# Kernel optimization log

Hardware: AMD Instinct MI355X
Metric: run time of the kernel (lower is better)

## Reference

```python
import jax, jax.numpy as jnp
import numpy as np

N_NODES = 50000
N_EDGES = 800000
IN_FEATS = 128
HIDDEN = 128
DNN_H = 256
N_CLASSES = 40


def setup_inputs() -> dict:
    key = jax.random.key(0)
    ks = jax.random.split(key, 12)
    features = jax.random.normal(ks[0], (N_NODES, IN_FEATS), dtype=jnp.float32)
    src = jax.random.randint(ks[1], (N_EDGES,), 0, N_NODES, dtype=jnp.int32)
    dst = jax.random.randint(ks[2], (N_EDGES,), 0, N_NODES, dtype=jnp.int32)
    def lin(k, fi, fo):
        s = 1.0 / np.sqrt(fi)
        return jax.random.uniform(k, (fi, fo), jnp.float32, -s, s)
    W1 = lin(ks[3], IN_FEATS, HIDDEN)
    b1 = jnp.zeros((HIDDEN,), jnp.float32)
    W2 = lin(ks[4], HIDDEN, HIDDEN)
    b2 = jnp.zeros((HIDDEN,), jnp.float32)
    Wd1 = lin(ks[5], HIDDEN, DNN_H)
    bd1 = jnp.zeros((DNN_H,), jnp.float32)
    Wd2 = lin(ks[6], DNN_H, N_CLASSES)
    bd2 = jnp.zeros((N_CLASSES,), jnp.float32)
    return {"features": features, "src": src, "dst": dst,
            "W1": W1, "b1": b1, "W2": W2, "b2": b2,
            "Wd1": Wd1, "bd1": bd1, "Wd2": Wd2, "bd2": bd2}


def _graph_conv(x, src, dst, W, b):
    # dgl GraphConv, norm='both': D_out^{-1/2} -> sum-aggregate -> D_in^{-1/2} -> linear -> relu
    ones = jnp.ones((src.shape[0],), x.dtype)
    deg_out = jax.ops.segment_sum(ones, src, num_segments=N_NODES)
    deg_in = jax.ops.segment_sum(ones, dst, num_segments=N_NODES)
    inv_sqrt_out = jax.lax.rsqrt(jnp.maximum(deg_out, 1.0))  # clamp zero-degree to 1 like dgl
    inv_sqrt_in = jax.lax.rsqrt(jnp.maximum(deg_in, 1.0))
    x = x * inv_sqrt_out[:, None]
    h = jax.ops.segment_sum(x[src], dst, num_segments=N_NODES)  # [N, d] sparse SpMM
    h = h * inv_sqrt_in[:, None]
    return jax.nn.relu(h @ W + b)


def reference(features, src, dst, W1, b1, W2, b2, Wd1, bd1, Wd2, bd2):
    h = _graph_conv(features, src, dst, W1, b1)   # dropout = identity (eval)
    h = _graph_conv(h, src, dst, W2, b2)
    # DNN: Linear -> LeakyReLU(0.01) -> (dropout identity), x2
    h = jax.nn.leaky_relu(h @ Wd1 + bd1, negative_slope=0.01)
    h = jax.nn.leaky_relu(h @ Wd2 + bd2, negative_slope=0.01)
    return h
```

## Files before the change

### kernel.cpp

```cpp
#include <hip/hip_runtime.h>


#define SCAN_B 256

typedef __attribute__((ext_vector_type(8))) short short8v;
typedef __attribute__((ext_vector_type(4))) float f32x4;

__global__ void k_scanA(const int* __restrict__ deg_in, int* __restrict__ incl,
                        int* __restrict__ bsum, int N) {
    __shared__ int s[SCAN_B];
    int t = threadIdx.x, i = blockIdx.x * SCAN_B + t;
    int v = (i < N) ? deg_in[i] : 0;
    s[t] = v; __syncthreads();
    for (int o = 1; o < SCAN_B; o <<= 1) {
        int x = (t >= o) ? s[t - o] : 0;
        __syncthreads();
        s[t] += x;
        __syncthreads();
    }
    if (i < N) incl[i] = s[t];
    if (t == SCAN_B - 1) bsum[blockIdx.x] = s[t];
}

__global__ void k_scanB(int* __restrict__ bsum, int NB) {
    __shared__ int s[SCAN_B];
    int t = threadIdx.x;
    int v = (t < NB) ? bsum[t] : 0;
    s[t] = v; __syncthreads();
    for (int o = 1; o < SCAN_B; o <<= 1) {
        int x = (t >= o) ? s[t - o] : 0;
        __syncthreads();
        s[t] += x;
        __syncthreads();
    }
    if (t < NB) bsum[t] = s[t] - v;
}

__global__ void k_scanC(const int* __restrict__ deg_in, const int* __restrict__ deg_out,
                        int* __restrict__ row_ptr, const int* __restrict__ bsum,
                        float* __restrict__ inv_in, float* __restrict__ inv_out,
                        int N, int E) {
    int t = threadIdx.x, i = blockIdx.x * SCAN_B + t;
    if (i < N) {
        int di = deg_in[i];
        row_ptr[i] = row_ptr[i] - di + bsum[blockIdx.x];
        inv_in[i]  = rsqrtf(fmaxf((float)di, 1.0f));
        inv_out[i] = rsqrtf(fmaxf((float)deg_out[i], 1.0f));
    }
    if (i == 0) row_ptr[N] = E;
}

__global__ void k_scatter3(const int* __restrict__ src, const int* __restrict__ dst,
                           const int* __restrict__ row_ptr, const int* __restrict__ rank,
                           const float* __restrict__ inv_out,
                           int2* __restrict__ edges, int E) {
    int i = blockIdx.x * blockDim.x + threadIdx.x;
    if (i < E) {
        int s = src[i];
        int2 p;
        p.x = s;
        p.y = __float_as_int(inv_out[s]);
        edges[row_ptr[dst[i]] + rank[i]] = p;
    }
}

__global__ void k_gather2(const float* __restrict__ X, const int2* __restrict__ edges,
                          const int* __restrict__ row_ptr, const float* __restrict__ inv_in,
                          const float* __restrict__ bias, float* __restrict__ Y, int N) {
    int lane = threadIdx.x & 31;
    int row = blockIdx.x * 8 + (threadIdx.x >> 5);
    if (row >= N) return;
    int rs = row_ptr[row], re = row_ptr[row + 1];
    float4 acc = {0.f, 0.f, 0.f, 0.f};
    int e = rs;
    #define LDROW(s) (*reinterpret_cast<const float4*>(&X[(size_t)(s) * 128 + lane * 4]))
    for (; e + 4 <= re; e += 4) {
        int2 p0 = edges[e], p1 = edges[e + 1], p2 = edges[e + 2], p3 = edges[e + 3];
        float4 x0 = LDROW(p0.x), x1 = LDROW(p1.x), x2 = LDROW(p2.x), x3 = LDROW(p3.x);
        float c0 = __int_as_float(p0.y), c1 = __int_as_float(p1.y);
        float c2 = __int_as_float(p2.y), c3 = __int_as_float(p3.y);
        acc.x += c0 * x0.x + c1 * x1.x + c2 * x2.x + c3 * x3.x;
        acc.y += c0 * x0.y + c1 * x1.y + c2 * x2.y + c3 * x3.y;
        acc.z += c0 * x0.z + c1 * x1.z + c2 * x2.z + c3 * x3.z;
        acc.w += c0 * x0.w + c1 * x1.w + c2 * x2.w + c3 * x3.w;
    }
    for (; e < re; ++e) {
        int2 p = edges[e];
        float c = __int_as_float(p.y);
        float4 xv = LDROW(p.x);
        acc.x += c * xv.x; acc.y += c * xv.y; acc.z += c * xv.z; acc.w += c * xv.w;
    }
    #undef LDROW
    float si = inv_in[row];
    float4 b4 = *reinterpret_cast<const float4*>(&bias[lane * 4]);
    float4 o;
    o.x = fmaxf(fmaf(acc.x, si, b4.x), 0.f);
    o.y = fmaxf(fmaf(acc.y, si, b4.y), 0.f);
    o.z = fmaxf(fmaf(acc.z, si, b4.z), 0.f);
    o.w = fmaxf(fmaf(acc.w, si, b4.w), 0.f);
    *reinterpret_cast<float4*>(&Y[(size_t)row * 128 + lane * 4]) = o;
}

__device__ inline unsigned short bf16_rne(float f) {
    unsigned int u = __float_as_uint(f);
    u += 0x7fffu + ((u >> 16) & 1u);
    return (unsigned short)(u >> 16);
}

__device__ inline void split1(float a, unsigned short& h, unsigned short& l) {
    unsigned short hh = bf16_rne(a);
    float hf = __uint_as_float((unsigned int)hh << 16);
    l = bf16_rne(a - hf);
    h = hh;
}

template<int K, int N, int ACT, bool DEG>
__global__ __launch_bounds__(256) void k_gemm_mfma(const float* __restrict__ A,
                                                   const float* __restrict__ W,
                                                   const float* __restrict__ bias,
                                                   float* __restrict__ C, int M,
                                                   const int* __restrict__ src,
                                                   const int* __restrict__ dst,
                                                   int* __restrict__ deg_out,
                                                   int* __restrict__ deg_in,
                                                   int* __restrict__ rank, int E, int epb,
                                                   int gmm, int degb) {
    __shared__ unsigned short Bh[64 * K], Bl[64 * K];
    __shared__ unsigned short Ah[128 * 32], Al[128 * 32];

    int t = threadIdx.x;
    int m0, cb;
    if (DEG) {
        int bid = blockIdx.x;
        if (bid < degb) {
            int base = bid * epb;
            int end = min(E, base + epb);
            for (int i = base + t; i < end; i += 256) {
                atomicAdd(&deg_out[src[i]], 1);
                rank[i] = atomicAdd(&deg_in[dst[i]], 1);
            }
            return;
        }
        int tile = bid - degb;
        m0 = (tile % gmm) * 128;
        cb = (tile / gmm) * 64;
    } else {
        m0 = blockIdx.x * 128;
        cb = blockIdx.y * 64;
    }

    {
        int c = t & 63;
        int kb = (t >> 6) * (K / 4);
        bool cok = (N % 64 == 0) || (cb + c < N);
        for (int j = 0; j < K / 4; ++j) {
            int k = kb + j;
            float v = cok ? W[(size_t)k * N + cb + c] : 0.f;
            unsigned short hi, lo; split1(v, hi, lo);
            int byte = (c * 2 * K + 2 * k) ^ ((c & 7) << 4);
            Bh[byte >> 1] = hi;
            Bl[byte >> 1] = lo;
        }
    }

    f32x4 acc[4][2];
    #pragma unroll
    for (int i = 0; i < 4; ++i)
        #pragma unroll
        for (int j = 0; j < 2; ++j)
            acc[i][j] = (f32x4){0.f, 0.f, 0.f, 0.f};

    int lane = t & 63;
    int wave = t >> 6;
    int wm = wave >> 1, wn = wave & 1;
    int lr = lane & 15, lg = lane >> 4;

    for (int kt = 0; kt < K / 32; ++kt) {
        __syncthreads();
        #pragma unroll
        for (int i = 0; i < 4; ++i) {
            int g = i * 256 + t;
            int r = g >> 3;
            int kq = (g & 7) * 4;
            int gr = m0 + r;
            float4 v = {0.f, 0.f, 0.f, 0.f};
            if (gr < M) v = *reinterpret_cast<const float4*>(&A[(size_t)gr * K + kt * 32 + kq]);
            ushort4 h4, l4;
            split1(v.x, h4.x, l4.x);
            split1(v.y, h4.y, l4.y);
            split1(v.z, h4.z, l4.z);
            split1(v.w, h4.w, l4.w);
            int byte = (r * 64 + 2 * kq) ^ ((r & 7) << 4);
            *reinterpret_cast<ushort4*>(&Ah[byte >> 1]) = h4;
            *reinterpret_cast<ushort4*>(&Al[byte >> 1]) = l4;
        }
        __syncthreads();

        short8v bhf[2], blf[2];
        #pragma unroll
        for (int nf = 0; nf < 2; ++nf) {
            int c = wn * 32 + nf * 16 + lr;
            int byte = (c * 2 * K + 2 * (kt * 32 + lg * 8)) ^ ((c & 7) << 4);
            bhf[nf] = *reinterpret_cast<const short8v*>(&Bh[byte >> 1]);
            blf[nf] = *reinterpret_cast<const short8v*>(&Bl[byte >> 1]);
        }
        #pragma unroll
        for (int mf = 0; mf < 4; ++mf) {
            int r = wm * 64 + mf * 16 + lr;
            int byte = (r * 64 + 2 * (lg * 8)) ^ ((r & 7) << 4);
            short8v ahf = *reinterpret_cast<const short8v*>(&Ah[byte >> 1]);
            short8v alf = *reinterpret_cast<const short8v*>(&Al[byte >> 1]);
            #pragma unroll
            for (int nf = 0; nf < 2; ++nf) {
                acc[mf][nf] = __builtin_amdgcn_mfma_f32_16x16x32_bf16(ahf, bhf[nf], acc[mf][nf], 0, 0, 0);
                acc[mf][nf] = __builtin_amdgcn_mfma_f32_16x16x32_bf16(ahf, blf[nf], acc[mf][nf], 0, 0, 0);
                acc[mf][nf] = __builtin_amdgcn_mfma_f32_16x16x32_bf16(alf, bhf[nf], acc[mf][nf], 0, 0, 0);
            }
        }
    }

    #pragma unroll
    for (int mf = 0; mf < 4; ++mf) {
        #pragma unroll
        for (int nf = 0; nf < 2; ++nf) {
            int col = cb + wn * 32 + nf * 16 + lr;
            if ((N % 64 != 0) && col >= N) continue;
            float bv = (ACT < 2) ? bias[col] : 0.f;
            #pragma unroll
            for (int rg = 0; rg < 4; ++rg) {
                int row = m0 + wm * 64 + mf * 16 + lg * 4 + rg;
                if (row < M) {
                    float v = acc[mf][nf][rg];
                    if (ACT == 0) v = fmaxf(v + bv, 0.f);
                    else if (ACT == 1) { v += bv; v = (v > 0.f) ? v : 0.01f * v; }
                    C[(size_t)row * N + col] = v;
                }
            }
        }
    }
}

extern "C" void kernel_launch(void* const* d_in, const int* in_sizes, int n_in,
                              void* d_out, int out_size, void* d_ws, size_t ws_size,
                              hipStream_t stream) {
    const float* feat = (const float*)d_in[0];
    const int*   src  = (const int*)d_in[1];
    const int*   dst  = (const int*)d_in[2];
    const float* W1   = (const float*)d_in[3];
    const float* b1   = (const float*)d_in[4];
    const float* W2   = (const float*)d_in[5];
    const float* b2   = (const float*)d_in[6];
    const float* Wd1  = (const float*)d_in[7];
    const float* bd1  = (const float*)d_in[8];
    const float* Wd2  = (const float*)d_in[9];
    const float* bd2  = (const float*)d_in[10];
    float* out = (float*)d_out;

    const int N = in_sizes[0] / 128;
    const int E = in_sizes[1];

    char* ws = (char*)d_ws;
    size_t off = 0;
    auto alloc = [&](size_t bytes) -> void* {
        void* p = ws + off;
        off += (bytes + 255) & ~(size_t)255;
        return p;
    };
    int* deg_out  = (int*)alloc((size_t)N * 4);
    int* deg_in   = (int*)alloc((size_t)N * 4);
    int* row_ptr  = (int*)alloc((size_t)(N + 1) * 4);
    int* bsum     = (int*)alloc(SCAN_B * 4);
    int* rank     = (int*)alloc((size_t)E * 4);
    int2* edges   = (int2*)alloc((size_t)E * 8);
    float* inv_out = (float*)alloc((size_t)N * 4);
    float* inv_in  = (float*)alloc((size_t)N * 4);
    float* bufA = (float*)alloc((size_t)N * 128 * 4);
    float* bufB = (float*)alloc((size_t)N * 128 * 4);
    float* hd   = (float*)alloc((size_t)N * 256 * 4);

    size_t zspan = (char*)deg_in + (size_t)N * 4 - (char*)deg_out;
    hipMemsetAsync(deg_out, 0, zspan, stream);

    int gE = (E + 255) / 256;
    int gN = (N + SCAN_B - 1) / SCAN_B;
    int gG = (N + 7) / 8;
    int gMM = (N + 127) / 128;

    const int DEGB = 512;
    int epb = (E + DEGB - 1) / DEGB;
    k_gemm_mfma<128, 128, 2, true><<<DEGB + gMM * 2, 256, 0, stream>>>(
        feat, W1, nullptr, bufA, N, src, dst, deg_out, deg_in, rank, E, epb, gMM, DEGB);

    k_scanA<<<gN, SCAN_B, 0, stream>>>(deg_in, row_ptr, bsum, N);
    k_scanB<<<1, SCAN_B, 0, stream>>>(bsum, gN);
    k_scanC<<<gN, SCAN_B, 0, stream>>>(deg_in, deg_out, row_ptr, bsum, inv_in, inv_out, N, E);
    k_scatter3<<<gE, 256, 0, stream>>>(src, dst, row_ptr, rank, inv_out, edges, E);

    k_gather2<<<gG, 256, 0, stream>>>(bufA, edges, row_ptr, inv_in, b1, bufB, N);
    k_gemm_mfma<128, 128, 2, false><<<dim3(gMM, 2), 256, 0, stream>>>(
        bufB, W2, nullptr, bufA, N, nullptr, nullptr, nullptr, nullptr, nullptr, 0, 0, 0, 0);
    k_gather2<<<gG, 256, 0, stream>>>(bufA, edges, row_ptr, inv_in, b2, bufB, N);
    k_gemm_mfma<128, 256, 1, false><<<dim3(gMM, 4), 256, 0, stream>>>(
        bufB, Wd1, bd1, hd, N, nullptr, nullptr, nullptr, nullptr, nullptr, 0, 0, 0, 0);
    k_gemm_mfma<256, 40, 1, false><<<dim3(gMM, 1), 256, 0, stream>>>(
        hd, Wd2, bd2, out, N, nullptr, nullptr, nullptr, nullptr, nullptr, 0, 0, 0, 0);
}
```

Before: 337.1 us.

## Unroll gather by eight, add wide-tile GEMM for Wd1, double degree blocks

The gather loop now handles eight edges per iteration, so more independent row loads are in flight per warp. A new GEMM kernel computes the 128-to-256 DNN layer with a 128x128 output tile per block and the whole weight slice staged in LDS as split bf16 hi/lo. This halves the grid in the column direction and reuses each A tile across more columns. The fused degree-counting launch also gets twice as many degree blocks, and the larger tiles raise LDS and register use, which may lower occupancy.

```diff
diff --git a/kernel.cpp b/kernel.cpp
--- a/kernel.cpp
+++ b/kernel.cpp
@@ -74,15 +74,29 @@
     float4 acc = {0.f, 0.f, 0.f, 0.f};
     int e = rs;
     #define LDROW(s) (*reinterpret_cast<const float4*>(&X[(size_t)(s) * 128 + lane * 4]))
+    for (; e + 8 <= re; e += 8) {
+        int2 p0 = edges[e],     p1 = edges[e + 1], p2 = edges[e + 2], p3 = edges[e + 3];
+        int2 p4 = edges[e + 4], p5 = edges[e + 5], p6 = edges[e + 6], p7 = edges[e + 7];
+        float4 x0 = LDROW(p0.x), x1 = LDROW(p1.x), x2 = LDROW(p2.x), x3 = LDROW(p3.x);
+        float4 x4 = LDROW(p4.x), x5 = LDROW(p5.x), x6 = LDROW(p6.x), x7 = LDROW(p7.x);
+        float c0 = __int_as_float(p0.y), c1 = __int_as_float(p1.y);
+        float c2 = __int_as_float(p2.y), c3 = __int_as_float(p3.y);
+        float c4 = __int_as_float(p4.y), c5 = __int_as_float(p5.y);
+        float c6 = __int_as_float(p6.y), c7 = __int_as_float(p7.y);
+        acc.x += c0*x0.x + c1*x1.x + c2*x2.x + c3*x3.x + c4*x4.x + c5*x5.x + c6*x6.x + c7*x7.x;
+        acc.y += c0*x0.y + c1*x1.y + c2*x2.y + c3*x3.y + c4*x4.y + c5*x5.y + c6*x6.y + c7*x7.y;
+        acc.z += c0*x0.z + c1*x1.z + c2*x2.z + c3*x3.z + c4*x4.z + c5*x5.z + c6*x6.z + c7*x7.z;
+        acc.w += c0*x0.w + c1*x1.w + c2*x2.w + c3*x3.w + c4*x4.w + c5*x5.w + c6*x6.w + c7*x7.w;
+    }
     for (; e + 4 <= re; e += 4) {
         int2 p0 = edges[e], p1 = edges[e + 1], p2 = edges[e + 2], p3 = edges[e + 3];
         float4 x0 = LDROW(p0.x), x1 = LDROW(p1.x), x2 = LDROW(p2.x), x3 = LDROW(p3.x);
         float c0 = __int_as_float(p0.y), c1 = __int_as_float(p1.y);
         float c2 = __int_as_float(p2.y), c3 = __int_as_float(p3.y);
-        acc.x += c0 * x0.x + c1 * x1.x + c2 * x2.x + c3 * x3.x;
-        acc.y += c0 * x0.y + c1 * x1.y + c2 * x2.y + c3 * x3.y;
-        acc.z += c0 * x0.z + c1 * x1.z + c2 * x2.z + c3 * x3.z;
-        acc.w += c0 * x0.w + c1 * x1.w + c2 * x2.w + c3 * x3.w;
+        acc.x += c0*x0.x + c1*x1.x + c2*x2.x + c3*x3.x;
+        acc.y += c0*x0.y + c1*x1.y + c2*x2.y + c3*x3.y;
+        acc.z += c0*x0.z + c1*x1.z + c2*x2.z + c3*x3.z;
+        acc.w += c0*x0.w + c1*x1.w + c2*x2.w + c3*x3.w;
     }
     for (; e < re; ++e) {
         int2 p = edges[e];
@@ -233,6 +247,108 @@
                     float v = acc[mf][nf][rg];
                     if (ACT == 0) v = fmaxf(v + bv, 0.f);
                     else if (ACT == 1) { v += bv; v = (v > 0.f) ? v : 0.01f * v; }
+                    C[(size_t)row * N + col] = v;
+                }
+            }
+        }
+    }
+}
+
+template<int N, int ACT>
+__global__ __launch_bounds__(256) void k_gemm_mfma_w(const float* __restrict__ A,
+                                                     const float* __restrict__ W,
+                                                     const float* __restrict__ bias,
+                                                     float* __restrict__ C, int M) {
+    constexpr int K = 128;
+    __shared__ unsigned short Bh[128 * K], Bl[128 * K];
+    __shared__ unsigned short Ah[128 * 32], Al[128 * 32];
+
+    int t = threadIdx.x;
+    int m0 = blockIdx.x * 128;
+    int cb = blockIdx.y * 128;
+
+    {
+        int c = t & 127;
+        int kb = (t >> 7) * (K / 2);
+        for (int j = 0; j < K / 2; ++j) {
+            int k = kb + j;
+            float v = W[(size_t)k * N + cb + c];
+            unsigned short hi, lo; split1(v, hi, lo);
+            int byte = (c * 2 * K + 2 * k) ^ ((c & 7) << 4);
+            Bh[byte >> 1] = hi;
+            Bl[byte >> 1] = lo;
+        }
+    }
+
+    f32x4 acc[4][4];
+    #pragma unroll
+    for (int i = 0; i < 4; ++i)
+        #pragma unroll
+        for (int j = 0; j < 4; ++j)
+            acc[i][j] = (f32x4){0.f, 0.f, 0.f, 0.f};
+
+    int lane = t & 63;
+    int wave = t >> 6;
+    int wm = wave >> 1, wn = wave & 1;
+    int lr = lane & 15, lg = lane >> 4;
+
+    for (int kt = 0; kt < K / 32; ++kt) {
+        __syncthreads();
+        #pragma unroll
+        for (int i = 0; i < 4; ++i) {
+            int g = i * 256 + t;
+            int r = g >> 3;
+            int kq = (g & 7) * 4;
+            int gr = m0 + r;
+            float4 v = {0.f, 0.f, 0.f, 0.f};
+            if (gr < M) v = *reinterpret_cast<const float4*>(&A[(size_t)gr * K + kt * 32 + kq]);
+            ushort4 h4, l4;
+            split1(v.x, h4.x, l4.x);
+            split1(v.y, h4.y, l4.y);
+            split1(v.z, h4.z, l4.z);
+            split1(v.w, h4.w, l4.w);
+            int byte = (r * 64 + 2 * kq) ^ ((r & 7) << 4);
+            *reinterpret_cast<ushort4*>(&Ah[byte >> 1]) = h4;
+            *reinterpret_cast<ushort4*>(&Al[byte >> 1]) = l4;
+        }
+        __syncthreads();
+
+        short8v bhf[4], blf[4];
+        #pragma unroll
+        for (int nf = 0; nf < 4; ++nf) {
+            int c = wn * 64 + nf * 16 + lr;
+            int byte = (c * 2 * K + 2 * (kt * 32 + lg * 8)) ^ ((c & 7) << 4);
+            bhf[nf] = *reinterpret_cast<const short8v*>(&Bh[byte >> 1]);
+            blf[nf] = *reinterpret_cast<const short8v*>(&Bl[byte >> 1]);
+        }
+        #pragma unroll
+        for (int mf = 0; mf < 4; ++mf) {
+            int r = wm * 64 + mf * 16 + lr;
+            int byte = (r * 64 + 2 * (lg * 8)) ^ ((r & 7) << 4);
+            short8v ahf = *reinterpret_cast<const short8v*>(&Ah[byte >> 1]);
+            short8v alf = *reinterpret_cast<const short8v*>(&Al[byte >> 1]);
+            #pragma unroll
+            for (int nf = 0; nf < 4; ++nf) {
+                acc[mf][nf] = __builtin_amdgcn_mfma_f32_16x16x32_bf16(ahf, bhf[nf], acc[mf][nf], 0, 0, 0);
+                acc[mf][nf] = __builtin_amdgcn_mfma_f32_16x16x32_bf16(ahf, blf[nf], acc[mf][nf], 0, 0, 0);
+                acc[mf][nf] = __builtin_amdgcn_mfma_f32_16x16x32_bf16(alf, bhf[nf], acc[mf][nf], 0, 0, 0);
+            }
+        }
+    }
+
+    #pragma unroll
+    for (int mf = 0; mf < 4; ++mf) {
+        #pragma unroll
+        for (int nf = 0; nf < 4; ++nf) {
+            int col = cb + wn * 64 + nf * 16 + lr;
+            float bv = bias[col];
+            #pragma unroll
+            for (int rg = 0; rg < 4; ++rg) {
+                int row = m0 + wm * 64 + mf * 16 + lg * 4 + rg;
+                if (row < M) {
+                    float v = acc[mf][nf][rg] + bv;
+                    if (ACT == 0) v = fmaxf(v, 0.f);
+                    else v = (v > 0.f) ? v : 0.01f * v;
                     C[(size_t)row * N + col] = v;
                 }
             }
@@ -286,7 +402,7 @@
     int gG = (N + 7) / 8;
     int gMM = (N + 127) / 128;
 
-    const int DEGB = 512;
+    const int DEGB = 1024;
     int epb = (E + DEGB - 1) / DEGB;
     k_gemm_mfma<128, 128, 2, true><<<DEGB + gMM * 2, 256, 0, stream>>>(
         feat, W1, nullptr, bufA, N, src, dst, deg_out, deg_in, rank, E, epb, gMM, DEGB);
@@ -300,8 +416,7 @@
     k_gemm_mfma<128, 128, 2, false><<<dim3(gMM, 2), 256, 0, stream>>>(
         bufB, W2, nullptr, bufA, N, nullptr, nullptr, nullptr, nullptr, nullptr, 0, 0, 0, 0);
     k_gather2<<<gG, 256, 0, stream>>>(bufA, edges, row_ptr, inv_in, b2, bufB, N);
-    k_gemm_mfma<128, 256, 1, false><<<dim3(gMM, 4), 256, 0, stream>>>(
-        bufB, Wd1, bd1, hd, N, nullptr, nullptr, nullptr, nullptr, nullptr, 0, 0, 0, 0);
+    k_gemm_mfma_w<256, 1><<<dim3(gMM, 2), 256, 0, stream>>>(bufB, Wd1, bd1, hd, N);
     k_gemm_mfma<256, 40, 1, false><<<dim3(gMM, 1), 256, 0, stream>>>(
         hd, Wd2, bd2, out, N, nullptr, nullptr, nullptr, nullptr, nullptr, 0, 0, 0, 0);
 }
```

Result: slower. 344.4 us (+2.2%).
